# Kernel optimization log

Hardware: AMD Instinct MI355X
Metric: run time of the kernel (lower is better)

Reference implementation:

```python
import jax, jax.numpy as jnp
import numpy as np

TEMP = 1.0


def _layernorm(x):
    # mean/std over last dim; torch.std is unbiased (ddof=1); no eps in original
    x = x - jnp.mean(x, axis=-1, keepdims=True)
    return x / jnp.std(x, axis=-1, keepdims=True, ddof=1)


def setup_inputs() -> dict:
    key = jax.random.key(0)
    ks = jax.random.split(key, 5)
    B, S, d_in, d = 8, 2048, 768, 1024
    return {
        "seq": jax.random.normal(ks[0], (B, S, d_in), dtype=jnp.float32),
        "embedding": jax.random.normal(ks[1], (d_in, d), dtype=jnp.float32),
        "W1": jax.random.normal(ks[2], (d, d), dtype=jnp.float32),
        "W2": jax.random.normal(ks[3], (d, d), dtype=jnp.float32),
        "readout": jax.random.normal(ks[4], (d,), dtype=jnp.float32),
    }


def reference(seq, embedding, W1, W2, readout):
    d_in = seq.shape[-1]
    d = embedding.shape[-1]
    x = jnp.matmul(seq, embedding) / jnp.sqrt(jnp.float32(d_in))  # [B,S,d]
    # depth == 1: single block
    gram = jnp.einsum("bsd,btd->bst", x, x) / x.shape[-1]  # [B,S,S]
    weights = jax.nn.softmax(gram / TEMP, axis=-1)
    post_attn = _layernorm(x + jnp.matmul(weights, x))  # [B,S,d]
    h = jnp.matmul(post_attn, W1) / jnp.sqrt(jnp.float32(d))
    h = jnp.matmul(jax.nn.relu(h), W2) / jnp.sqrt(jnp.float32(d))
    x = _layernorm(h + post_attn)
    pooled = jnp.mean(x, axis=1)  # [B,d]
    out = jnp.matmul(pooled, readout) / jnp.sqrt(jnp.float32(d))  # [B]
    return out
```

## Files before the change

### kernel.cpp

```cpp
#include <hip/hip_runtime.h>
#include <hip/hip_bf16.h>

typedef __bf16 bf16x8 __attribute__((ext_vector_type(8)));
typedef float f32x4 __attribute__((ext_vector_type(4)));

__device__ __forceinline__ unsigned short f2bf(float f) {
  union { float f; unsigned u; } x; x.f = f;
  unsigned r = x.u + 0x7fffu + ((x.u >> 16) & 1u);
  return (unsigned short)(r >> 16);
}
__device__ __forceinline__ float bf2f(unsigned short u) {
  union { unsigned u; float f; } x; x.u = (unsigned)u << 16;
  return x.f;
}
__device__ __forceinline__ unsigned short f2h(float f) {
  union { _Float16 h; unsigned short u; } x; x.h = (_Float16)f;
  return x.u;
}
__device__ __forceinline__ float h2f(unsigned short u) {
  union { _Float16 h; unsigned short u; } x; x.u = u;
  return (float)x.h;
}

__device__ __forceinline__ void async_ld16(const void* g, void* l) {
  __builtin_amdgcn_global_load_lds(
      (__attribute__((address_space(1))) void*)const_cast<void*>(g),
      (__attribute__((address_space(3))) void*)l, 16, 0, 0);
}


#define EPI_F32    0
#define EPI_BF     1
#define EPI_RELUBF 2
#define EPI_F16    3

__global__ __launch_bounds__(512, 2) void gemm_bt(
    const unsigned short* __restrict__ A,
    const unsigned short* __restrict__ Bt,
    int M, int N, int K, int nbatch,
    long sA, long sB, long sC,
    float scale, int mode, void* __restrict__ outp)
{
  __shared__ unsigned short lds[65536];
  const int t = threadIdx.x;
  const int w = t >> 6, l = t & 63;
  const int lr = l & 15, lg = l >> 4;
  const int wr = w >> 2, wc = w & 3;
  const int ntn = N >> 8;
  const int tiles = (M >> 8) * ntn;
  const int chunk = (tiles * nbatch) >> 3;
  const int bid = blockIdx.x;
  const int wg = (bid & 7) * chunk + (bid >> 3);
  const int batch = wg / tiles;
  const int rem = wg - batch * tiles;
  const int row0 = (rem / ntn) << 8;
  const int col0 = (rem % ntn) << 8;

  const unsigned short* Ab  = A  + (long)batch * sA;
  const unsigned short* Btb = Bt + (long)batch * sB;

  const int ks = ((lg ^ ((lr >> 1) & 3)) << 3);

  const int srow = w * 16 + (l >> 2);
  const int kgo  = (((l & 3) ^ ((l >> 3) & 3)) << 3);
  const long aoff0 = (long)(row0 + srow) * K + kgo;
  const long boff0 = (long)(col0 + srow) * K + kgo;
  const long off128 = (long)K << 7;

  const int NT = K >> 6;

#define STAGEP(partE, base, kcol)                                      \
  { async_ld16((base) + (kcol),          &lds[(partE) + t * 8]);       \
    async_ld16((base) + off128 + (kcol), &lds[(partE) + 4096 + t * 8]); }

  f32x4 acc[8][4];
#pragma unroll
  for (int m = 0; m < 8; ++m)
#pragma unroll
    for (int n = 0; n < 4; ++n) acc[m][n] = (f32x4){0.f, 0.f, 0.f, 0.f};

  STAGEP(0,     Btb + boff0, 0);
  STAGEP(8192,  Ab + aoff0,  0);
  STAGEP(16384, Btb + boff0, 32);
  STAGEP(24576, Ab + aoff0,  32);
  __builtin_amdgcn_sched_barrier(0);

  for (int tt = 0; tt < NT; ++tt) {
    const int bufe  = (tt & 1) << 15;
    const int nbufe = ((tt + 1) & 1) << 15;
    const bool st = (tt + 1) < NT;
    const int kn = (tt + 1) << 6;

#pragma unroll
    for (int kh = 0; kh < 2; ++kh) {
      if (kh == 0 || st) { asm volatile("s_waitcnt vmcnt(4)" ::: "memory"); }
      else               { asm volatile("s_waitcnt vmcnt(0)" ::: "memory"); }
      __builtin_amdgcn_sched_barrier(0);
      __builtin_amdgcn_s_barrier();
      __builtin_amdgcn_sched_barrier(0);

      const int pB = bufe + kh * 16384;
      const int pA = pB + 8192;

      bf16x8 bfr[4];
#pragma unroll
      for (int nf = 0; nf < 4; ++nf) {
        int rb = wc * 64 + nf * 16 + lr;
        bfr[nf] = *(const bf16x8*)&lds[pB + rb * 32 + ks];
      }
      {
        bf16x8 af[4];
#pragma unroll
        for (int i = 0; i < 4; ++i) {
          int ra = wr * 128 + i * 16 + lr;
          af[i] = *(const bf16x8*)&lds[pA + ra * 32 + ks];
        }
        if (st) STAGEP(nbufe + kh * 16384, Btb + boff0, kn + kh * 32);
        __builtin_amdgcn_s_setprio(1);
#pragma unroll
        for (int i = 0; i < 4; ++i)
#pragma unroll
          for (int nf = 0; nf < 4; ++nf)
            acc[i][nf] = __builtin_amdgcn_mfma_f32_16x16x32_bf16(af[i], bfr[nf], acc[i][nf], 0, 0, 0);
        __builtin_amdgcn_s_setprio(0);
      }
      {
        bf16x8 af[4];
#pragma unroll
        for (int i = 0; i < 4; ++i) {
          int ra = wr * 128 + 64 + i * 16 + lr;
          af[i] = *(const bf16x8*)&lds[pA + ra * 32 + ks];
        }
        if (st) STAGEP(nbufe + kh * 16384 + 8192, Ab + aoff0, kn + kh * 32);
        __builtin_amdgcn_s_setprio(1);
#pragma unroll
        for (int i = 0; i < 4; ++i)
#pragma unroll
          for (int nf = 0; nf < 4; ++nf)
            acc[4 + i][nf] = __builtin_amdgcn_mfma_f32_16x16x32_bf16(af[i], bfr[nf], acc[4 + i][nf], 0, 0, 0);
        __builtin_amdgcn_s_setprio(0);
      }
      __builtin_amdgcn_sched_barrier(0);
    }
  }

  float* outF = (float*)outp;
  unsigned short* outH = (unsigned short*)outp;
  const size_t cb = (size_t)batch * (size_t)sC;
#pragma unroll
  for (int mf = 0; mf < 8; ++mf) {
    int rbase = row0 + wr * 128 + mf * 16 + lg * 4;
#pragma unroll
    for (int nf = 0; nf < 4; ++nf) {
      int c = col0 + wc * 64 + nf * 16 + lr;
      f32x4 v = acc[mf][nf];
#pragma unroll
      for (int q = 0; q < 4; ++q) {
        size_t idx = cb + (size_t)(rbase + q) * N + c;
        float val = v[q] * scale;
        if (mode == EPI_F32)         outF[idx] = val;
        else if (mode == EPI_BF)     outH[idx] = f2bf(val);
        else if (mode == EPI_RELUBF) outH[idx] = f2bf(fmaxf(val, 0.f));
        else                         outH[idx] = f2h(val);
      }
    }
  }
#undef STAGEP
}


__device__ __forceinline__ float wave_sum(float v) {
#pragma unroll
  for (int o = 32; o; o >>= 1) v += __shfl_xor(v, o, 64);
  return v;
}
__device__ __forceinline__ float wave_max(float v) {
#pragma unroll
  for (int o = 32; o; o >>= 1) v = fmaxf(v, __shfl_xor(v, o, 64));
  return v;
}

__global__ __launch_bounds__(256) void cast_bf16(const float* __restrict__ in,
                                                 unsigned short* __restrict__ out, long n) {
  long i = ((long)blockIdx.x * 256 + threadIdx.x) * 4;
  if (i >= n) return;
  float4 v = *(const float4*)&in[i];
  ushort4 o;
  o.x = f2bf(v.x); o.y = f2bf(v.y); o.z = f2bf(v.z); o.w = f2bf(v.w);
  *(ushort4*)&out[i] = o;
}

__global__ __launch_bounds__(256) void transpose_cast(const float* __restrict__ in,
                                                      unsigned short* __restrict__ out,
                                                      int R, int C) {
  __shared__ float tile[32][33];
  int c0 = blockIdx.x * 32, r0 = blockIdx.y * 32;
  int tx = threadIdx.x, ty = threadIdx.y;
  for (int i = ty; i < 32; i += 8) tile[i][tx] = in[(size_t)(r0 + i) * C + c0 + tx];
  __syncthreads();
  for (int i = ty; i < 32; i += 8) out[(size_t)(c0 + i) * R + r0 + tx] = f2bf(tile[tx][i]);
}

__global__ __launch_bounds__(256) void transpose_b16(const unsigned short* __restrict__ in,
                                                     unsigned short* __restrict__ out,
                                                     int R, int C) {
  __shared__ unsigned short tile[32][33];
  int c0 = blockIdx.x * 32, r0 = blockIdx.y * 32;
  size_t zb = (size_t)blockIdx.z * R * C;
  int tx = threadIdx.x, ty = threadIdx.y;
  for (int i = ty; i < 32; i += 8) tile[i][tx] = in[zb + (size_t)(r0 + i) * C + c0 + tx];
  __syncthreads();
  for (int i = ty; i < 32; i += 8) out[zb + (size_t)(c0 + i) * R + r0 + tx] = tile[tx][i];
}

__global__ __launch_bounds__(256) void softmax_rows(const unsigned short* __restrict__ g,
                                                    unsigned short* __restrict__ wout) {
  __shared__ float red[4];
  int row = blockIdx.x, t = threadIdx.x;
  const unsigned short* gr = g + ((size_t)row << 11) + t * 8;
  ushort4 ua = *(const ushort4*)gr;
  ushort4 ub = *(const ushort4*)(gr + 4);
  float a0 = h2f(ua.x), a1 = h2f(ua.y), a2 = h2f(ua.z), a3 = h2f(ua.w);
  float b0 = h2f(ub.x), b1 = h2f(ub.y), b2 = h2f(ub.z), b3 = h2f(ub.w);
  float mx = fmaxf(fmaxf(fmaxf(a0, a1), fmaxf(a2, a3)),
                   fmaxf(fmaxf(b0, b1), fmaxf(b2, b3)));
  mx = wave_max(mx);
  if ((t & 63) == 0) red[t >> 6] = mx;
  __syncthreads();
  mx = fmaxf(fmaxf(red[0], red[1]), fmaxf(red[2], red[3]));
  float e0 = __expf(a0 - mx), e1 = __expf(a1 - mx), e2 = __expf(a2 - mx), e3 = __expf(a3 - mx);
  float e4 = __expf(b0 - mx), e5 = __expf(b1 - mx), e6 = __expf(b2 - mx), e7 = __expf(b3 - mx);
  float s = ((e0 + e1) + (e2 + e3)) + ((e4 + e5) + (e6 + e7));
  s = wave_sum(s);
  __syncthreads();
  if ((t & 63) == 0) red[t >> 6] = s;
  __syncthreads();
  s = (red[0] + red[1]) + (red[2] + red[3]);
  float inv = 1.0f / s;
  ushort4 o0, o1;
  o0.x = f2bf(e0 * inv); o0.y = f2bf(e1 * inv); o0.z = f2bf(e2 * inv); o0.w = f2bf(e3 * inv);
  o1.x = f2bf(e4 * inv); o1.y = f2bf(e5 * inv); o1.z = f2bf(e6 * inv); o1.w = f2bf(e7 * inv);
  size_t base = ((size_t)row << 11) + t * 8;
  *(ushort4*)&wout[base] = o0;
  *(ushort4*)&wout[base + 4] = o1;
}

__global__ __launch_bounds__(256) void ln_residual_bf(const unsigned short* __restrict__ xb,
                                                      const float* __restrict__ attn,
                                                      unsigned short* __restrict__ outB) {
  __shared__ float red[4];
  int row = blockIdx.x, t = threadIdx.x;
  size_t base = ((size_t)row << 10) + t * 4;
  ushort4 ua = *(const ushort4*)&xb[base];
  float4 vb = *(const float4*)&attn[base];
  float4 v = {bf2f(ua.x) + vb.x, bf2f(ua.y) + vb.y, bf2f(ua.z) + vb.z, bf2f(ua.w) + vb.w};
  float s = (v.x + v.y) + (v.z + v.w);
  float ss = (v.x * v.x + v.y * v.y) + (v.z * v.z + v.w * v.w);
  s = wave_sum(s);
  if ((t & 63) == 0) red[t >> 6] = s;
  __syncthreads();
  s = (red[0] + red[1]) + (red[2] + red[3]);
  ss = wave_sum(ss);
  __syncthreads();
  if ((t & 63) == 0) red[t >> 6] = ss;
  __syncthreads();
  ss = (red[0] + red[1]) + (red[2] + red[3]);
  float mean = s * (1.0f / 1024.0f);
  float var = (ss - s * mean) * (1.0f / 1023.0f);
  float rstd = rsqrtf(var);
  ushort4 ob;
  ob.x = f2bf((v.x - mean) * rstd); ob.y = f2bf((v.y - mean) * rstd);
  ob.z = f2bf((v.z - mean) * rstd); ob.w = f2bf((v.w - mean) * rstd);
  *(ushort4*)&outB[base] = ob;
}

__global__ __launch_bounds__(256) void ln_residual_dot(const unsigned short* __restrict__ h2,
                                                       const unsigned short* __restrict__ post,
                                                       const float* __restrict__ readout,
                                                       float* __restrict__ rowdot) {
  __shared__ float red[4];
  int row = blockIdx.x, t = threadIdx.x;
  size_t base = ((size_t)row << 10) + t * 4;
  ushort4 ua = *(const ushort4*)&h2[base];
  ushort4 ub = *(const ushort4*)&post[base];
  float4 v = {bf2f(ua.x) + bf2f(ub.x), bf2f(ua.y) + bf2f(ub.y),
              bf2f(ua.z) + bf2f(ub.z), bf2f(ua.w) + bf2f(ub.w)};
  float s = (v.x + v.y) + (v.z + v.w);
  float ss = (v.x * v.x + v.y * v.y) + (v.z * v.z + v.w * v.w);
  s = wave_sum(s);
  if ((t & 63) == 0) red[t >> 6] = s;
  __syncthreads();
  s = (red[0] + red[1]) + (red[2] + red[3]);
  ss = wave_sum(ss);
  __syncthreads();
  if ((t & 63) == 0) red[t >> 6] = ss;
  __syncthreads();
  ss = (red[0] + red[1]) + (red[2] + red[3]);
  float mean = s * (1.0f / 1024.0f);
  float var = (ss - s * mean) * (1.0f / 1023.0f);
  float rstd = rsqrtf(var);
  float4 r = *(const float4*)&readout[t * 4];
  float dot = (v.x - mean) * rstd * r.x + (v.y - mean) * rstd * r.y +
              (v.z - mean) * rstd * r.z + (v.w - mean) * rstd * r.w;
  dot = wave_sum(dot);
  __syncthreads();
  if ((t & 63) == 0) red[t >> 6] = dot;
  __syncthreads();
  if (t == 0) rowdot[row] = (red[0] + red[1]) + (red[2] + red[3]);
}

__global__ __launch_bounds__(256) void reduce_out(const float* __restrict__ rowdot,
                                                  float* __restrict__ out) {
  __shared__ float red[4];
  int b = blockIdx.x, t = threadIdx.x;
  float s = 0.f;
  for (int i = t; i < 2048; i += 256) s += rowdot[(size_t)b * 2048 + i];
  s = wave_sum(s);
  if ((t & 63) == 0) red[t >> 6] = s;
  __syncthreads();
  if (t == 0) out[b] = ((red[0] + red[1]) + (red[2] + red[3])) * (1.0f / 65536.0f);
}

extern "C" void kernel_launch(void* const* d_in, const int* in_sizes, int n_in,
                              void* d_out, int out_size, void* d_ws, size_t ws_size,
                              hipStream_t stream) {
  const float* seq     = (const float*)d_in[0];
  const float* emb     = (const float*)d_in[1];
  const float* W1      = (const float*)d_in[2];
  const float* W2      = (const float*)d_in[3];
  const float* readout = (const float*)d_in[4];
  float* out = (float*)d_out;

  char* ws = (char*)d_ws;
  const size_t MB = 1024u * 1024u;
  unsigned short* x_b    = (unsigned short*)(ws + 0);
  unsigned short* h2b    = (unsigned short*)(ws + 0);
  unsigned short* xT     = (unsigned short*)(ws + 32 * MB);
  unsigned short* hrelu  = (unsigned short*)(ws + 32 * MB);
  unsigned short* gram   = (unsigned short*)(ws + 64 * MB);
  float*          attn   = (float*)(ws + 64 * MB);
  unsigned short* wts    = (unsigned short*)(ws + 128 * MB);
  unsigned short* post_b = (unsigned short*)(ws + 128 * MB);
  unsigned short* seq_b  = (unsigned short*)(ws + 192 * MB);
  unsigned short* embT   = (unsigned short*)(ws + 216 * MB);
  unsigned short* W1T    = (unsigned short*)(ws + 218 * MB);
  unsigned short* W2T    = (unsigned short*)(ws + 220 * MB);
  float*          rowdot = (float*)(ws + 222 * MB);

  cast_bf16<<<12288, 256, 0, stream>>>(seq, seq_b, 12582912L);
  transpose_cast<<<dim3(32, 24), dim3(32, 8), 0, stream>>>(emb, embT, 768, 1024);
  transpose_cast<<<dim3(32, 32), dim3(32, 8), 0, stream>>>(W1, W1T, 1024, 1024);
  transpose_cast<<<dim3(32, 32), dim3(32, 8), 0, stream>>>(W2, W2T, 1024, 1024);

  gemm_bt<<<256, 512, 0, stream>>>(seq_b, embT, 16384, 1024, 768, 1, 0, 0, 0,
                                   0.03608439182435161f, EPI_BF, x_b);

  transpose_b16<<<dim3(32, 64, 8), dim3(32, 8), 0, stream>>>(x_b, xT, 2048, 1024);

  gemm_bt<<<512, 512, 0, stream>>>(x_b, x_b, 2048, 2048, 1024, 8,
                                   2048L * 1024, 2048L * 1024, 2048L * 2048,
                                   1.0f / 1024.0f, EPI_F16, gram);

  softmax_rows<<<16384, 256, 0, stream>>>(gram, wts);

  gemm_bt<<<256, 512, 0, stream>>>(wts, xT, 2048, 1024, 2048, 8,
                                   2048L * 2048, 1024L * 2048, 2048L * 1024,
                                   1.0f, EPI_F32, attn);

  ln_residual_bf<<<16384, 256, 0, stream>>>(x_b, attn, post_b);

  gemm_bt<<<256, 512, 0, stream>>>(post_b, W1T, 16384, 1024, 1024, 1, 0, 0, 0,
                                   0.03125f, EPI_RELUBF, hrelu);
  gemm_bt<<<256, 512, 0, stream>>>(hrelu, W2T, 16384, 1024, 1024, 1, 0, 0, 0,
                                   0.03125f, EPI_BF, h2b);

  ln_residual_dot<<<16384, 256, 0, stream>>>(h2b, post_b, readout, rowdot);
  reduce_out<<<8, 256, 0, stream>>>(rowdot, out);
}
```

Before: 385.2 us.

## Exploit Gram matrix symmetry and store attention output in bf16

Adds a dedicated gram_sym kernel that computes only the upper-triangular 256x256 tiles of each batch's X·X^T (36 tiles per batch instead of 64) and writes each off-diagonal tile twice, once directly and once transposed into the mirrored position. Separately, the weights·x GEMM now writes bf16 instead of fp32, and the layernorm-residual kernel reads bf16 for both inputs. Together these cut matmul FLOPs for the Gram step and halve the traffic of the attention intermediate. In exchange, the mirrored stores are strided ushort4 writes, the 288-block grid may load-balance unevenly, and the attention output loses precision before the layernorm.

```diff
diff --git a/kernel.cpp b/kernel.cpp
--- a/kernel.cpp
+++ b/kernel.cpp
@@ -168,6 +168,134 @@
 #undef STAGEP
 }
 
+__global__ __launch_bounds__(512, 2) void gram_sym(
+    const unsigned short* __restrict__ X,
+    unsigned short* __restrict__ outH)
+{
+  __shared__ unsigned short lds[65536];
+  const int t = threadIdx.x;
+  const int w = t >> 6, l = t & 63;
+  const int lr = l & 15, lg = l >> 4;
+  const int wr = w >> 2, wc = w & 3;
+  const int bid = blockIdx.x;
+  const int wg = (bid & 7) * 36 + (bid >> 3);
+  const int batch = wg / 36;
+  int r8 = wg - batch * 36;
+  int bi = 0;
+  while (r8 >= 8 - bi) { r8 -= 8 - bi; ++bi; }
+  const int bj = bi + r8;
+  const int row0 = bi << 8;
+  const int col0 = bj << 8;
+
+  const unsigned short* Xb = X + (long)batch * 2048 * 1024;
+
+  const int ks = ((lg ^ ((lr >> 1) & 3)) << 3);
+  const int srow = w * 16 + (l >> 2);
+  const int kgo  = (((l & 3) ^ ((l >> 3) & 3)) << 3);
+  const long aoff0 = (long)(row0 + srow) * 1024 + kgo;
+  const long boff0 = (long)(col0 + srow) * 1024 + kgo;
+  const long off128 = 1024L << 7;
+
+#define STAGEP(partE, base, kcol)                                      \
+  { async_ld16((base) + (kcol),          &lds[(partE) + t * 8]);       \
+    async_ld16((base) + off128 + (kcol), &lds[(partE) + 4096 + t * 8]); }
+
+  f32x4 acc[8][4];
+#pragma unroll
+  for (int m = 0; m < 8; ++m)
+#pragma unroll
+    for (int n = 0; n < 4; ++n) acc[m][n] = (f32x4){0.f, 0.f, 0.f, 0.f};
+
+  STAGEP(0,     Xb + boff0, 0);
+  STAGEP(8192,  Xb + aoff0,  0);
+  STAGEP(16384, Xb + boff0, 32);
+  STAGEP(24576, Xb + aoff0,  32);
+  __builtin_amdgcn_sched_barrier(0);
+
+  for (int tt = 0; tt < 16; ++tt) {
+    const int bufe  = (tt & 1) << 15;
+    const int nbufe = ((tt + 1) & 1) << 15;
+    const bool st = (tt + 1) < 16;
+    const int kn = (tt + 1) << 6;
+
+#pragma unroll
+    for (int kh = 0; kh < 2; ++kh) {
+      if (kh == 0 || st) { asm volatile("s_waitcnt vmcnt(4)" ::: "memory"); }
+      else               { asm volatile("s_waitcnt vmcnt(0)" ::: "memory"); }
+      __builtin_amdgcn_sched_barrier(0);
+      __builtin_amdgcn_s_barrier();
+      __builtin_amdgcn_sched_barrier(0);
+
+      const int pB = bufe + kh * 16384;
+      const int pA = pB + 8192;
+
+      bf16x8 bfr[4];
+#pragma unroll
+      for (int nf = 0; nf < 4; ++nf) {
+        int rb = wc * 64 + nf * 16 + lr;
+        bfr[nf] = *(const bf16x8*)&lds[pB + rb * 32 + ks];
+      }
+      {
+        bf16x8 af[4];
+#pragma unroll
+        for (int i = 0; i < 4; ++i) {
+          int ra = wr * 128 + i * 16 + lr;
+          af[i] = *(const bf16x8*)&lds[pA + ra * 32 + ks];
+        }
+        if (st) STAGEP(nbufe + kh * 16384, Xb + boff0, kn + kh * 32);
+        __builtin_amdgcn_s_setprio(1);
+#pragma unroll
+        for (int i = 0; i < 4; ++i)
+#pragma unroll
+          for (int nf = 0; nf < 4; ++nf)
+            acc[i][nf] = __builtin_amdgcn_mfma_f32_16x16x32_bf16(af[i], bfr[nf], acc[i][nf], 0, 0, 0);
+        __builtin_amdgcn_s_setprio(0);
+      }
+      {
+        bf16x8 af[4];
+#pragma unroll
+        for (int i = 0; i < 4; ++i) {
+          int ra = wr * 128 + 64 + i * 16 + lr;
+          af[i] = *(const bf16x8*)&lds[pA + ra * 32 + ks];
+        }
+        if (st) STAGEP(nbufe + kh * 16384 + 8192, Xb + aoff0, kn + kh * 32);
+        __builtin_amdgcn_s_setprio(1);
+#pragma unroll
+        for (int i = 0; i < 4; ++i)
+#pragma unroll
+          for (int nf = 0; nf < 4; ++nf)
+            acc[4 + i][nf] = __builtin_amdgcn_mfma_f32_16x16x32_bf16(af[i], bfr[nf], acc[4 + i][nf], 0, 0, 0);
+        __builtin_amdgcn_s_setprio(0);
+      }
+      __builtin_amdgcn_sched_barrier(0);
+    }
+  }
+
+  unsigned short* ob = outH + (size_t)batch * 2048 * 2048;
+  const float scale = 1.0f / 1024.0f;
+  const bool mirror = (bi != bj);
+#pragma unroll
+  for (int mf = 0; mf < 8; ++mf) {
+    int rbase = row0 + wr * 128 + mf * 16 + lg * 4;
+#pragma unroll
+    for (int nf = 0; nf < 4; ++nf) {
+      int c = col0 + wc * 64 + nf * 16 + lr;
+      f32x4 v = acc[mf][nf];
+      unsigned short h0 = f2h(v[0] * scale), h1 = f2h(v[1] * scale);
+      unsigned short h2 = f2h(v[2] * scale), h3 = f2h(v[3] * scale);
+      ob[(size_t)(rbase + 0) * 2048 + c] = h0;
+      ob[(size_t)(rbase + 1) * 2048 + c] = h1;
+      ob[(size_t)(rbase + 2) * 2048 + c] = h2;
+      ob[(size_t)(rbase + 3) * 2048 + c] = h3;
+      if (mirror) {
+        ushort4 m4 = {h0, h1, h2, h3};
+        *(ushort4*)&ob[(size_t)c * 2048 + rbase] = m4;
+      }
+    }
+  }
+#undef STAGEP
+}
+
 
 __device__ __forceinline__ float wave_sum(float v) {
 #pragma unroll
@@ -245,15 +373,16 @@
   *(ushort4*)&wout[base + 4] = o1;
 }
 
-__global__ __launch_bounds__(256) void ln_residual_bf(const unsigned short* __restrict__ xb,
-                                                      const float* __restrict__ attn,
+__global__ __launch_bounds__(256) void ln_residual_bb(const unsigned short* __restrict__ xb,
+                                                      const unsigned short* __restrict__ ab,
                                                       unsigned short* __restrict__ outB) {
   __shared__ float red[4];
   int row = blockIdx.x, t = threadIdx.x;
   size_t base = ((size_t)row << 10) + t * 4;
   ushort4 ua = *(const ushort4*)&xb[base];
-  float4 vb = *(const float4*)&attn[base];
-  float4 v = {bf2f(ua.x) + vb.x, bf2f(ua.y) + vb.y, bf2f(ua.z) + vb.z, bf2f(ua.w) + vb.w};
+  ushort4 ub = *(const ushort4*)&ab[base];
+  float4 v = {bf2f(ua.x) + bf2f(ub.x), bf2f(ua.y) + bf2f(ub.y),
+              bf2f(ua.z) + bf2f(ub.z), bf2f(ua.w) + bf2f(ub.w)};
   float s = (v.x + v.y) + (v.z + v.w);
   float ss = (v.x * v.x + v.y * v.y) + (v.z * v.z + v.w * v.w);
   s = wave_sum(s);
@@ -338,7 +467,7 @@
   unsigned short* xT     = (unsigned short*)(ws + 32 * MB);
   unsigned short* hrelu  = (unsigned short*)(ws + 32 * MB);
   unsigned short* gram   = (unsigned short*)(ws + 64 * MB);
-  float*          attn   = (float*)(ws + 64 * MB);
+  unsigned short* attn_b = (unsigned short*)(ws + 64 * MB);
   unsigned short* wts    = (unsigned short*)(ws + 128 * MB);
   unsigned short* post_b = (unsigned short*)(ws + 128 * MB);
   unsigned short* seq_b  = (unsigned short*)(ws + 192 * MB);
@@ -357,17 +486,15 @@
 
   transpose_b16<<<dim3(32, 64, 8), dim3(32, 8), 0, stream>>>(x_b, xT, 2048, 1024);
 
-  gemm_bt<<<512, 512, 0, stream>>>(x_b, x_b, 2048, 2048, 1024, 8,
-                                   2048L * 1024, 2048L * 1024, 2048L * 2048,
-                                   1.0f / 1024.0f, EPI_F16, gram);
+  gram_sym<<<288, 512, 0, stream>>>(x_b, gram);
 
   softmax_rows<<<16384, 256, 0, stream>>>(gram, wts);
 
   gemm_bt<<<256, 512, 0, stream>>>(wts, xT, 2048, 1024, 2048, 8,
                                    2048L * 2048, 1024L * 2048, 2048L * 1024,
-                                   1.0f, EPI_F32, attn);
-
-  ln_residual_bf<<<16384, 256, 0, stream>>>(x_b, attn, post_b);
+                                   1.0f, EPI_BF, attn_b);
+
+  ln_residual_bb<<<16384, 256, 0, stream>>>(x_b, attn_b, post_b);
 
   gemm_bt<<<256, 512, 0, stream>>>(post_b, W1T, 16384, 1024, 1024, 1, 0, 0, 0,
                                    0.03125f, EPI_RELUBF, hrelu);
```

Result: faster. 368.5 us (-4.3%).
